# Performance work log

Measured on AMD Instinct MI355X. Metric: run time of the kernel, lower is better.

The kernel has to match this reference:

```python
import jax, jax.numpy as jnp
import numpy as np
from jax import lax

H = 39  # hidden size == input feature size (hardcoded in the torch module)


def _lstm_scan(xs, W_ih, W_hh, b_ih, b_hh):
    """Run a unidirectional LSTM over xs: (T, B, I) -> (T, B, H).
    PyTorch gate order: i, f, g, o."""
    T, B, _ = xs.shape
    # Precompute input projections for all timesteps: (T, B, 4H)
    pre = jnp.einsum('tbi,gi->tbg', xs, W_ih) + b_ih + b_hh
    h0 = jnp.zeros((B, H), dtype=xs.dtype)
    c0 = jnp.zeros((B, H), dtype=xs.dtype)

    def step(carry, g_in):
        h, c = carry
        g = g_in + h @ W_hh.T  # (B, 4H)
        i, f, gg, o = jnp.split(g, 4, axis=-1)
        i = jax.nn.sigmoid(i)
        f = jax.nn.sigmoid(f)
        gg = jnp.tanh(gg)
        o = jax.nn.sigmoid(o)
        c = f * c + i * gg
        h = o * jnp.tanh(c)
        return (h, c), h

    _, hs = lax.scan(step, (h0, c0), pre)
    return hs  # (T, B, H)


def setup_inputs() -> dict:
    key = jax.random.key(0)
    ks = jax.random.split(key, 9)
    B, T = 512, 2048
    s = 1.0 / np.sqrt(H)
    x = jax.random.normal(ks[0], (B, T * H), dtype=jnp.float32)
    def w(k, shape):
        return jax.random.uniform(k, shape, dtype=jnp.float32, minval=-s, maxval=s)
    return {
        'x': x,
        'W_ih_f': w(ks[1], (4 * H, H)),
        'W_hh_f': w(ks[2], (4 * H, H)),
        'b_ih_f': w(ks[3], (4 * H,)),
        'b_hh_f': w(ks[4], (4 * H,)),
        'W_ih_b': w(ks[5], (4 * H, H)),
        'W_hh_b': w(ks[6], (4 * H, H)),
        'b_ih_b': w(ks[7], (4 * H,)),
        'b_hh_b': w(ks[8], (4 * H,)),
    }


def reference(x, W_ih_f, W_hh_f, b_ih_f, b_hh_f, W_ih_b, W_hh_b, b_ih_b, b_hh_b):
    B = x.shape[0]
    T = x.shape[1] // H
    xs = jnp.swapaxes(x.reshape(B, T, H), 0, 1)  # (T, B, H)

    h_f = _lstm_scan(xs, W_ih_f, W_hh_f, b_ih_f, b_hh_f)          # forward dir, time order
    h_b_rev = _lstm_scan(xs[::-1], W_ih_b, W_hh_b, b_ih_b, b_hh_b)  # backward dir, processing order
    # torch output for backward dir is h_b_rev flipped to time order; the module then
    # flips it again along time before concat -> equals h_b_rev directly.
    out = jnp.concatenate([h_f, h_b_rev], axis=-1)  # (T, B, 2H)
    out = jnp.swapaxes(out, 0, 1).reshape(B, T * 2 * H)
    return out
```

## Files before the change

### kernel.cpp

```cpp
#include <hip/hip_runtime.h>
#include <math.h>

#define H   39
#define G4  156
#define TL  2048
#define BB  512

__global__ __launch_bounds__(320, 5)
void lstm_bidir_kernel(const float* __restrict__ x,
                       const float* __restrict__ W_ih_f, const float* __restrict__ W_hh_f,
                       const float* __restrict__ b_ih_f, const float* __restrict__ b_hh_f,
                       const float* __restrict__ W_ih_b, const float* __restrict__ W_hh_b,
                       const float* __restrict__ b_ih_b, const float* __restrict__ b_hh_b,
                       float* __restrict__ out)
{
    const int blk = blockIdx.x;
    const int b   = blk >> 1;
    const int dir = blk & 1;
    const int tid = threadIdx.x;
    const int j   = tid >> 1;
    const int p   = tid & 1;
    const bool rowActive = (tid < 2 * G4);

    const float* __restrict__ W_ih = dir ? W_ih_b : W_ih_f;
    const float* __restrict__ W_hh = dir ? W_hh_b : W_hh_f;
    const float* __restrict__ b_ih = dir ? b_ih_b : b_ih_f;
    const float* __restrict__ b_hh = dir ? b_hh_b : b_hh_f;

    __shared__ __align__(16) float xbf[40];
    __shared__ __align__(16) float hbf[40];
    __shared__ float gates[G4];
    float4* xb4 = (float4*)xbf;
    float4* hb4 = (float4*)hbf;

    float4 wih[5], whh[5];
    float bias = 0.0f;
    if (rowActive) {
        #pragma unroll
        for (int m = 0; m < 5; ++m) {
            const int k0 = 8 * m + 4 * p;
            float a[4], h[4];
            #pragma unroll
            for (int e = 0; e < 4; ++e) {
                const int k = k0 + e;
                a[e] = (k < H) ? W_ih[j * H + k] : 0.0f;
                h[e] = (k < H) ? W_hh[j * H + k] : 0.0f;
            }
            wih[m] = make_float4(a[0], a[1], a[2], a[3]);
            whh[m] = make_float4(h[0], h[1], h[2], h[3]);
        }
        bias = b_ih[j] + b_hh[j];
    }
    const bool  isg  = (j >= 2 * H) && (j < 3 * H);
    const float amul = isg ? 2.0f : 1.0f;
    const float aoff = isg ? -1.0f : 0.0f;

    const float* __restrict__ xrow = x + (size_t)b * (TL * H);
    float* __restrict__ orow = out + (size_t)b * (TL * 2 * H) + dir * H;

    float c = 0.0f;
    if (tid < 40) {
        hbf[tid] = 0.0f;
        const int t0 = dir ? (TL - 1) : 0;
        xbf[tid] = (tid < H) ? xrow[(size_t)t0 * H + tid] : 0.0f;
    }
    __syncthreads();

    for (int s = 0; s < TL; ++s) {
        float xnext = 0.0f;
        if (tid < H && (s + 1) < TL) {
            const int tn = dir ? (TL - 2 - s) : (s + 1);
            xnext = xrow[(size_t)tn * H + tid];
        }

        if (rowActive) {
            float4 acc = make_float4(0.0f, 0.0f, 0.0f, 0.0f);
            #pragma unroll
            for (int m = 0; m < 5; ++m) {
                const int ci = 2 * m + p;
                const float4 xv = xb4[ci];
                const float4 hv = hb4[ci];
                acc.x = fmaf(wih[m].x, xv.x, fmaf(whh[m].x, hv.x, acc.x));
                acc.y = fmaf(wih[m].y, xv.y, fmaf(whh[m].y, hv.y, acc.y));
                acc.z = fmaf(wih[m].z, xv.z, fmaf(whh[m].z, hv.z, acc.z));
                acc.w = fmaf(wih[m].w, xv.w, fmaf(whh[m].w, hv.w, acc.w));
            }
            float psum = (acc.x + acc.y) + (acc.z + acc.w);
            const float tot  = psum + __shfl_xor(psum, 1) + bias;
            const float targ = amul * tot;
            const float e    = __expf(-targ);
            const float sg   = __builtin_amdgcn_rcpf(1.0f + e);
            const float act  = fmaf(amul, sg, aoff);
            if (p == 0) gates[j] = act;
        }
        __syncthreads();

        if (tid < H) {
            const float ig = gates[tid];
            const float fg = gates[H + tid];
            const float gg = gates[2 * H + tid];
            const float og = gates[3 * H + tid];
            c = fmaf(fg, c, ig * gg);
            const float e2 = __expf(-2.0f * c);
            const float th = fmaf(2.0f, __builtin_amdgcn_rcpf(1.0f + e2), -1.0f);
            const float h  = og * th;
            hbf[tid] = h;
            xbf[tid] = xnext;
            orow[(size_t)s * (2 * H) + tid] = h;
        }
        __syncthreads();
    }
}

extern "C" void kernel_launch(void* const* d_in, const int* in_sizes, int n_in,
                              void* d_out, int out_size, void* d_ws, size_t ws_size,
                              hipStream_t stream) {
    const float* x      = (const float*)d_in[0];
    const float* W_ih_f = (const float*)d_in[1];
    const float* W_hh_f = (const float*)d_in[2];
    const float* b_ih_f = (const float*)d_in[3];
    const float* b_hh_f = (const float*)d_in[4];
    const float* W_ih_b = (const float*)d_in[5];
    const float* W_hh_b = (const float*)d_in[6];
    const float* b_ih_b = (const float*)d_in[7];
    const float* b_hh_b = (const float*)d_in[8];
    float* out = (float*)d_out;

    dim3 grid(BB * 2);
    dim3 block(320);
    lstm_bidir_kernel<<<grid, block, 0, stream>>>(
        x, W_ih_f, W_hh_f, b_ih_f, b_hh_f,
        W_ih_b, W_hh_b, b_ih_b, b_hh_b, out);
}
```

Before: 1.907 ms.

## Group each hidden unit's four gates in one wave and double-buffer state

Threads are remapped so that the four gate rows of a hidden unit sit in the same 8-lane group of a wavefront. The gate values are then exchanged with shuffles instead of through shared memory. The h and x buffers are double-buffered, so each timestep needs one barrier instead of two. In exchange every lane redundantly computes the cell update, and some lanes in the last wave are idle.

```diff
diff --git a/kernel.cpp b/kernel.cpp
--- a/kernel.cpp
+++ b/kernel.cpp
@@ -18,96 +18,104 @@
     const int b   = blk >> 1;
     const int dir = blk & 1;
     const int tid = threadIdx.x;
-    const int j   = tid >> 1;
-    const int p   = tid & 1;
-    const bool rowActive = (tid < 2 * G4);
+    const int wav = tid >> 6;
+    const int lan = tid & 63;
+    const int nl  = lan >> 3;
+    const int g   = (lan >> 1) & 3;
+    const int p   = lan & 1;
+    const int n   = (wav << 3) + nl;
+    const bool nv = (n < H);
+    const int j   = g * H + n;
 
     const float* __restrict__ W_ih = dir ? W_ih_b : W_ih_f;
     const float* __restrict__ W_hh = dir ? W_hh_b : W_hh_f;
     const float* __restrict__ b_ih = dir ? b_ih_b : b_ih_f;
     const float* __restrict__ b_hh = dir ? b_hh_b : b_hh_f;
 
-    __shared__ __align__(16) float xbf[40];
-    __shared__ __align__(16) float hbf[40];
-    __shared__ float gates[G4];
-    float4* xb4 = (float4*)xbf;
-    float4* hb4 = (float4*)hbf;
+    __shared__ __align__(16) float xb[2][40];
+    __shared__ __align__(16) float hb[2][40];
 
     float4 wih[5], whh[5];
     float bias = 0.0f;
-    if (rowActive) {
+    #pragma unroll
+    for (int m = 0; m < 5; ++m) {
+        const int k0 = 8 * m + 4 * p;
+        float a[4], hh[4];
         #pragma unroll
-        for (int m = 0; m < 5; ++m) {
-            const int k0 = 8 * m + 4 * p;
-            float a[4], h[4];
-            #pragma unroll
-            for (int e = 0; e < 4; ++e) {
-                const int k = k0 + e;
-                a[e] = (k < H) ? W_ih[j * H + k] : 0.0f;
-                h[e] = (k < H) ? W_hh[j * H + k] : 0.0f;
-            }
-            wih[m] = make_float4(a[0], a[1], a[2], a[3]);
-            whh[m] = make_float4(h[0], h[1], h[2], h[3]);
+        for (int e = 0; e < 4; ++e) {
+            const int k = k0 + e;
+            const bool kv = nv && (k < H);
+            a[e]  = kv ? W_ih[j * H + k] : 0.0f;
+            hh[e] = kv ? W_hh[j * H + k] : 0.0f;
         }
-        bias = b_ih[j] + b_hh[j];
+        wih[m] = make_float4(a[0], a[1], a[2], a[3]);
+        whh[m] = make_float4(hh[0], hh[1], hh[2], hh[3]);
     }
-    const bool  isg  = (j >= 2 * H) && (j < 3 * H);
-    const float amul = isg ? 2.0f : 1.0f;
-    const float aoff = isg ? -1.0f : 0.0f;
+    if (nv) bias = b_ih[j] + b_hh[j];
+
+    const float amul = (g == 2) ? 2.0f : 1.0f;
+    const float aoff = (g == 2) ? -1.0f : 0.0f;
 
     const float* __restrict__ xrow = x + (size_t)b * (TL * H);
     float* __restrict__ orow = out + (size_t)b * (TL * 2 * H) + dir * H;
 
-    float c = 0.0f;
     if (tid < 40) {
-        hbf[tid] = 0.0f;
+        hb[0][tid] = 0.0f;
+        hb[1][tid] = 0.0f;
+        xb[1][tid] = 0.0f;
         const int t0 = dir ? (TL - 1) : 0;
-        xbf[tid] = (tid < H) ? xrow[(size_t)t0 * H + tid] : 0.0f;
+        xb[0][tid] = (tid < H) ? xrow[(size_t)t0 * H + tid] : 0.0f;
     }
     __syncthreads();
 
+    float c = 0.0f;
+    const bool hwr = (g == 0) && (p == 0) && nv;
+    const bool xld = (g == 1) && (p == 0) && nv;
+    const bool ost = (g == 2) && (p == 0) && nv;
+
     for (int s = 0; s < TL; ++s) {
+        const int cur = s & 1, nxt = cur ^ 1;
+
         float xnext = 0.0f;
-        if (tid < H && (s + 1) < TL) {
+        if (xld && (s + 1) < TL) {
             const int tn = dir ? (TL - 2 - s) : (s + 1);
-            xnext = xrow[(size_t)tn * H + tid];
+            xnext = xrow[(size_t)tn * H + n];
         }
 
-        if (rowActive) {
-            float4 acc = make_float4(0.0f, 0.0f, 0.0f, 0.0f);
-            #pragma unroll
-            for (int m = 0; m < 5; ++m) {
-                const int ci = 2 * m + p;
-                const float4 xv = xb4[ci];
-                const float4 hv = hb4[ci];
-                acc.x = fmaf(wih[m].x, xv.x, fmaf(whh[m].x, hv.x, acc.x));
-                acc.y = fmaf(wih[m].y, xv.y, fmaf(whh[m].y, hv.y, acc.y));
-                acc.z = fmaf(wih[m].z, xv.z, fmaf(whh[m].z, hv.z, acc.z));
-                acc.w = fmaf(wih[m].w, xv.w, fmaf(whh[m].w, hv.w, acc.w));
-            }
-            float psum = (acc.x + acc.y) + (acc.z + acc.w);
-            const float tot  = psum + __shfl_xor(psum, 1) + bias;
-            const float targ = amul * tot;
-            const float e    = __expf(-targ);
-            const float sg   = __builtin_amdgcn_rcpf(1.0f + e);
-            const float act  = fmaf(amul, sg, aoff);
-            if (p == 0) gates[j] = act;
+        const float4* xb4 = (const float4*)xb[cur];
+        const float4* hb4 = (const float4*)hb[cur];
+        float4 acc = make_float4(0.0f, 0.0f, 0.0f, 0.0f);
+        #pragma unroll
+        for (int m = 0; m < 5; ++m) {
+            const int ci = 2 * m + p;
+            const float4 xv = xb4[ci];
+            const float4 hv = hb4[ci];
+            acc.x = fmaf(wih[m].x, xv.x, fmaf(whh[m].x, hv.x, acc.x));
+            acc.y = fmaf(wih[m].y, xv.y, fmaf(whh[m].y, hv.y, acc.y));
+            acc.z = fmaf(wih[m].z, xv.z, fmaf(whh[m].z, hv.z, acc.z));
+            acc.w = fmaf(wih[m].w, xv.w, fmaf(whh[m].w, hv.w, acc.w));
         }
-        __syncthreads();
+        float psum = (acc.x + acc.y) + (acc.z + acc.w);
+        const float tot  = psum + __shfl_xor(psum, 1) + bias;
+        const float targ = amul * tot;
+        const float e    = __expf(-targ);
+        const float act  = fmaf(amul, __builtin_amdgcn_rcpf(1.0f + e), aoff);
 
-        if (tid < H) {
-            const float ig = gates[tid];
-            const float fg = gates[H + tid];
-            const float gg = gates[2 * H + tid];
-            const float og = gates[3 * H + tid];
-            c = fmaf(fg, c, ig * gg);
-            const float e2 = __expf(-2.0f * c);
-            const float th = fmaf(2.0f, __builtin_amdgcn_rcpf(1.0f + e2), -1.0f);
-            const float h  = og * th;
-            hbf[tid] = h;
-            xbf[tid] = xnext;
-            orow[(size_t)s * (2 * H) + tid] = h;
-        }
+        const int base = lan & ~7;
+        const float ig = __shfl(act, base + 0);
+        const float fg = __shfl(act, base + 2);
+        const float gg = __shfl(act, base + 4);
+        const float og = __shfl(act, base + 6);
+
+        c = fmaf(fg, c, ig * gg);
+        const float e2 = __expf(-2.0f * c);
+        const float th = fmaf(2.0f, __builtin_amdgcn_rcpf(1.0f + e2), -1.0f);
+        const float h  = og * th;
+
+        if (hwr) hb[nxt][n] = h;
+        if (xld) xb[nxt][n] = xnext;
+        if (ost) orow[(size_t)s * (2 * H) + n] = h;
+
         __syncthreads();
     }
 }
```

New measurement: 2.474 ms. +29.7%, slower.

## Split LSTM into input-projection precompute and register-resident recurrent kernel

Applied to the files above, without the earlier changes.

Adds a separate kernel that computes the input projections W_ih·x plus bias for chunks of timesteps into workspace. The recurrent kernel then holds W_hh rows in registers and broadcasts h through readlane instead of shared-memory vector loads, which removes half the per-step FMAs and the pair shuffle from the serial loop. Time is processed in chunks sized to the workspace, with h and c carried across launches through a state buffer. The cost is extra global traffic for the precomputed gates and several kernel launches, and the old fused kernel is kept as a fallback when workspace is too small.

```diff
diff --git a/kernel.cpp b/kernel.cpp
--- a/kernel.cpp
+++ b/kernel.cpp
@@ -6,13 +6,154 @@
 #define TL  2048
 #define BB  512
 
+__global__ __launch_bounds__(192)
+void lstm_pre_kernel(const float* __restrict__ x,
+                     const float* __restrict__ W_ih_f, const float* __restrict__ b_ih_f,
+                     const float* __restrict__ b_hh_f,
+                     const float* __restrict__ W_ih_b, const float* __restrict__ b_ih_b,
+                     const float* __restrict__ b_hh_b,
+                     float* __restrict__ pre, int t0, int SP, int lsp)
+{
+    const int dir = blockIdx.y;
+    const int j   = threadIdx.x;
+    const float* __restrict__ W_ih = dir ? W_ih_b : W_ih_f;
+    const float* __restrict__ b_i  = dir ? b_ih_b : b_ih_f;
+    const float* __restrict__ b_h  = dir ? b_hh_b : b_hh_f;
+
+    float wih[H];
+    float bias = 0.0f;
+    if (j < G4) {
+        #pragma unroll
+        for (int k = 0; k < H; ++k) wih[k] = W_ih[j * H + k];
+        bias = b_i[j] + b_h[j];
+    } else {
+        #pragma unroll
+        for (int k = 0; k < H; ++k) wih[k] = 0.0f;
+    }
+
+    const int r0 = blockIdx.x * 256;
+    for (int rr = 0; rr < 256; ++rr) {
+        const int r  = r0 + rr;
+        const int b  = r >> lsp;
+        const int ss = r & (SP - 1);
+        const int s  = t0 + ss;
+        const int tx = dir ? (TL - 1 - s) : s;
+        const float* __restrict__ xr = x + ((size_t)b * TL + tx) * H;
+        float a0 = bias, a1 = 0.0f, a2 = 0.0f;
+        #pragma unroll
+        for (int k = 0; k < 39; k += 3) {
+            a0 = fmaf(wih[k],     xr[k],     a0);
+            a1 = fmaf(wih[k + 1], xr[k + 1], a1);
+            a2 = fmaf(wih[k + 2], xr[k + 2], a2);
+        }
+        if (j < G4)
+            pre[((size_t)(b * 2 + dir) * SP + ss) * G4 + j] = a0 + (a1 + a2);
+    }
+}
+
+__global__ __launch_bounds__(192)
+void lstm_rec_kernel(const float* __restrict__ pre,
+                     const float* __restrict__ W_hh_f, const float* __restrict__ W_hh_b,
+                     float* __restrict__ out, float* __restrict__ state,
+                     int t0, int SP)
+{
+    const int blk = blockIdx.x;
+    const int b   = blk >> 1;
+    const int dir = blk & 1;
+    const int tid = threadIdx.x;
+    const int lan = tid & 63;
+    const int wav = tid >> 6;
+    const int j   = tid;
+
+    const float* __restrict__ W_hh = dir ? W_hh_b : W_hh_f;
+
+    __shared__ float gates[2][192];
+
+    float whh[H];
+    if (j < G4) {
+        #pragma unroll
+        for (int k = 0; k < H; ++k) whh[k] = W_hh[j * H + k];
+    } else {
+        #pragma unroll
+        for (int k = 0; k < H; ++k) whh[k] = 0.0f;
+    }
+    const bool  isg  = (j >= 2 * H) && (j < 3 * H);
+    const float amul = isg ? 2.0f : 1.0f;
+    const float aoff = isg ? -1.0f : 0.0f;
+
+    const float* __restrict__ prow = pre + (size_t)(b * 2 + dir) * SP * G4;
+    float* __restrict__ orow = out + (size_t)b * (TL * 2 * H) + dir * H;
+    float* __restrict__ st   = state + blk * 80;
+
+    float c  = 0.0f;
+    float hv = 0.0f;
+    if (t0 != 0 && lan < H) {
+        hv = st[lan];
+        c  = st[40 + lan];
+    }
+    int sh[H];
+    {
+        const int hb = __float_as_int(hv);
+        #pragma unroll
+        for (int k = 0; k < H; ++k) sh[k] = __builtin_amdgcn_readlane(hb, k);
+    }
+
+    float pv = (j < G4) ? prow[j] : 0.0f;
+
+    for (int ss = 0; ss < SP; ++ss) {
+        float pn = 0.0f;
+        if (j < G4 && (ss + 1) < SP) pn = prow[(size_t)(ss + 1) * G4 + j];
+
+        if (j < G4) {
+            float a0 = pv, a1 = 0.0f, a2 = 0.0f;
+            #pragma unroll
+            for (int k = 0; k < 39; k += 3) {
+                a0 = fmaf(whh[k],     __int_as_float(sh[k]),     a0);
+                a1 = fmaf(whh[k + 1], __int_as_float(sh[k + 1]), a1);
+                a2 = fmaf(whh[k + 2], __int_as_float(sh[k + 2]), a2);
+            }
+            const float tot  = a0 + (a1 + a2);
+            const float targ = amul * tot;
+            const float act  = fmaf(amul,
+                                    __builtin_amdgcn_rcpf(1.0f + __expf(-targ)),
+                                    aoff);
+            gates[ss & 1][j] = act;
+        }
+        __syncthreads();
+
+        if (lan < H) {
+            const float* g = gates[ss & 1];
+            const float ig = g[lan];
+            const float fg = g[H + lan];
+            const float gg = g[2 * H + lan];
+            const float og = g[3 * H + lan];
+            c = fmaf(fg, c, ig * gg);
+            const float e2 = __expf(-2.0f * c);
+            const float th = fmaf(2.0f, __builtin_amdgcn_rcpf(1.0f + e2), -1.0f);
+            hv = og * th;
+            if (wav == 0) orow[(size_t)(t0 + ss) * (2 * H) + lan] = hv;
+        }
+        {
+            const int hb = __float_as_int(hv);
+            #pragma unroll
+            for (int k = 0; k < H; ++k) sh[k] = __builtin_amdgcn_readlane(hb, k);
+        }
+        pv = pn;
+    }
+
+    if (wav == 0 && lan < H) {
+        st[lan]      = hv;
+        st[40 + lan] = c;
+    }
+}
+
 __global__ __launch_bounds__(320, 5)
-void lstm_bidir_kernel(const float* __restrict__ x,
-                       const float* __restrict__ W_ih_f, const float* __restrict__ W_hh_f,
-                       const float* __restrict__ b_ih_f, const float* __restrict__ b_hh_f,
-                       const float* __restrict__ W_ih_b, const float* __restrict__ W_hh_b,
-                       const float* __restrict__ b_ih_b, const float* __restrict__ b_hh_b,
-                       float* __restrict__ out)
+void lstm_bidir_fallback(const float* __restrict__ x,
+                         const float* __restrict__ W_ih_f, const float* __restrict__ W_hh_f,
+                         const float* __restrict__ b_ih_f, const float* __restrict__ b_hh_f,
+                         const float* __restrict__ W_ih_b, const float* __restrict__ W_hh_b,
+                         const float* __restrict__ b_ih_b, const float* __restrict__ b_hh_b,
+                         float* __restrict__ out)
 {
     const int blk = blockIdx.x;
     const int b   = blk >> 1;
@@ -39,15 +180,15 @@
         #pragma unroll
         for (int m = 0; m < 5; ++m) {
             const int k0 = 8 * m + 4 * p;
-            float a[4], h[4];
+            float a[4], hh[4];
             #pragma unroll
             for (int e = 0; e < 4; ++e) {
                 const int k = k0 + e;
-                a[e] = (k < H) ? W_ih[j * H + k] : 0.0f;
-                h[e] = (k < H) ? W_hh[j * H + k] : 0.0f;
+                a[e]  = (k < H) ? W_ih[j * H + k] : 0.0f;
+                hh[e] = (k < H) ? W_hh[j * H + k] : 0.0f;
             }
             wih[m] = make_float4(a[0], a[1], a[2], a[3]);
-            whh[m] = make_float4(h[0], h[1], h[2], h[3]);
+            whh[m] = make_float4(hh[0], hh[1], hh[2], hh[3]);
         }
         bias = b_ih[j] + b_hh[j];
     }
@@ -72,7 +213,6 @@
             const int tn = dir ? (TL - 2 - s) : (s + 1);
             xnext = xrow[(size_t)tn * H + tid];
         }
-
         if (rowActive) {
             float4 acc = make_float4(0.0f, 0.0f, 0.0f, 0.0f);
             #pragma unroll
@@ -89,12 +229,10 @@
             const float tot  = psum + __shfl_xor(psum, 1) + bias;
             const float targ = amul * tot;
             const float e    = __expf(-targ);
-            const float sg   = __builtin_amdgcn_rcpf(1.0f + e);
-            const float act  = fmaf(amul, sg, aoff);
+            const float act  = fmaf(amul, __builtin_amdgcn_rcpf(1.0f + e), aoff);
             if (p == 0) gates[j] = act;
         }
         __syncthreads();
-
         if (tid < H) {
             const float ig = gates[tid];
             const float fg = gates[H + tid];
@@ -126,9 +264,29 @@
     const float* b_hh_b = (const float*)d_in[8];
     float* out = (float*)d_out;
 
-    dim3 grid(BB * 2);
-    dim3 block(320);
-    lstm_bidir_kernel<<<grid, block, 0, stream>>>(
-        x, W_ih_f, W_hh_f, b_ih_f, b_hh_f,
-        W_ih_b, W_hh_b, b_ih_b, b_hh_b, out);
-}
+    int SP = TL;
+    while (SP >= 32) {
+        const size_t need = (size_t)(1 << 20)
+                          + (size_t)BB * 2 * SP * G4 * sizeof(float);
+        if (need <= ws_size) break;
+        SP >>= 1;
+    }
+
+    if (d_ws != nullptr && SP >= 32) {
+        float* state = (float*)d_ws;
+        float* pre   = (float*)((char*)d_ws + (1 << 20));
+        const int lsp = __builtin_ctz((unsigned)SP);
+        for (int t0 = 0; t0 < TL; t0 += SP) {
+            dim3 g1(2 * SP, 2);
+            lstm_pre_kernel<<<g1, 192, 0, stream>>>(
+                x, W_ih_f, b_ih_f, b_hh_f, W_ih_b, b_ih_b, b_hh_b,
+                pre, t0, SP, lsp);
+            lstm_rec_kernel<<<BB * 2, 192, 0, stream>>>(
+                pre, W_hh_f, W_hh_b, out, state, t0, SP);
+        }
+    } else {
+        lstm_bidir_fallback<<<BB * 2, 320, 0, stream>>>(
+            x, W_ih_f, W_hh_f, b_ih_f, b_hh_f,
+            W_ih_b, W_hh_b, b_ih_b, b_hh_b, out);
+    }
+}
```

New measurement: 3.583 ms. 87.9% more time.
